# Optimization experiments

Measured on AMD Instinct MI355X. Metric: run time of the kernel, lower is better.

Reference implementation:

```python
import jax, jax.numpy as jnp
import numpy as np

B = 512          # batch
IN_UNITS = 8     # primary capsule dim
IN_CH = 1152     # number of primary capsules
NUM_UNITS = 10   # output capsules (classes)
UNIT_SIZE = 16   # output capsule dim
BETA = 1.45      # squash beta: 1.45 - 0.22*(ep_iter/total) with ep_iter = n_iter = 0
NUM_ROUTING = 3


def setup_inputs() -> dict:
    key = jax.random.key(0)
    k1, k2 = jax.random.split(key)
    x = jax.random.normal(k1, (B, IN_UNITS, IN_CH), dtype=jnp.float32)
    # W parameter: torch shape (1, in_channels, num_units, unit_size, in_units); drop leading 1
    W = jax.random.normal(k2, (IN_CH, NUM_UNITS, UNIT_SIZE, IN_UNITS), dtype=jnp.float32)
    return {"x": x, "W": W}


def _squash(s):
    # s: (B, num_units, unit_size). Torch squash sums dim=2 of (B,1,nu,us,1),
    # which is the num_units axis (axis=1 here). Faithful to source.
    mag_sq = jnp.sum(s * s, axis=1, keepdims=True)          # (B,1,us)
    mag = jnp.sqrt(mag_sq)
    return mag_sq / (BETA + mag_sq) * (s / mag)


def reference(x, W):
    # u_hat[b,i,j,u] = sum_k W[i,j,u,k] * x[b,k,i]
    u_hat = jnp.einsum('ijuk,bki->biju', W, x)               # (B, IN_CH, NUM_UNITS, UNIT_SIZE)
    b_ij = jnp.zeros((IN_CH, NUM_UNITS), dtype=x.dtype)
    v = None
    for _ in range(NUM_ROUTING):
        c = jax.nn.softmax(b_ij, axis=0)                     # softmax over in_channels (dim=1 in torch)
        s = jnp.einsum('ij,biju->bju', c, u_hat)             # (B, NUM_UNITS, UNIT_SIZE)
        v = _squash(s)
        # b update: agreement <u_hat, v>, averaged over batch
        b_ij = jnp.einsum('biju,bju->ij', u_hat, v) / u_hat.shape[0]
    # rearrange 'b c (g h) w -> b c g (h w)' with g=4, w=1 -> reshape (B, nu, 4, us//4)
    return v.reshape(v.shape[0], NUM_UNITS, 4, UNIT_SIZE // 4)
```

## Files before the change

### kernel.cpp

```cpp
#include <hip/hip_runtime.h>
#include <hip/hip_bf16.h>
#include <math.h>

#define B    512
#define INU  8
#define IC   1152
#define NU   10
#define US   16
#define JU   160
#define KI   9216
#define BETAC 1.45f
#define NSPLIT 32
#define KC 288

typedef __attribute__((ext_vector_type(8))) __bf16 bf16x8;
typedef __attribute__((ext_vector_type(4))) float floatx4;

static __device__ __forceinline__ unsigned short f2bf(float f) {
  unsigned u = __builtin_bit_cast(unsigned, f);
  u = (u + 0x7fffu + ((u >> 16) & 1u)) >> 16;
  return (unsigned short)u;
}
static __device__ __forceinline__ float bf2f(unsigned short h) {
  return __builtin_bit_cast(float, ((unsigned)h) << 16);
}
static __device__ __forceinline__ uint4 scale8(uint4 wv, float4 cA, float4 cB) {
  union { uint4 u; unsigned short s[8]; } in;
  in.u = wv;
  union { uint4 u; __hip_bfloat162 h[4]; } o;
  o.h[0] = __float22bfloat162_rn(make_float2(bf2f(in.s[0]) * cA.x, bf2f(in.s[1]) * cA.y));
  o.h[1] = __float22bfloat162_rn(make_float2(bf2f(in.s[2]) * cA.z, bf2f(in.s[3]) * cA.w));
  o.h[2] = __float22bfloat162_rn(make_float2(bf2f(in.s[4]) * cB.x, bf2f(in.s[5]) * cB.y));
  o.h[3] = __float22bfloat162_rn(make_float2(bf2f(in.s[6]) * cB.z, bf2f(in.s[7]) * cB.w));
  return o.u;
}

__global__ __launch_bounds__(256) void prep_kernel(
    const float* __restrict__ x, const float* __restrict__ W,
    unsigned short* __restrict__ xb, unsigned short* __restrict__ xT,
    unsigned short* __restrict__ Wt, unsigned short* __restrict__ Wc,
    float* __restrict__ Wr) {
  __shared__ float ts[32 * 322];
  int id = blockIdx.x;
  int t = threadIdx.x;
  if (id < 1152) {
    int k0 = (id % 144) * 64;
    int b0 = (id / 144) * 64;
#pragma unroll
    for (int r = 0; r < 16; ++r) {
      int idx = t + 256 * r;
      int br = idx >> 6, kc = idx & 63;
      float v = x[(size_t)(b0 + br) * KI + k0 + kc];
      ts[br * 65 + kc] = v;
      xb[(size_t)(b0 + br) * KI + k0 + kc] = f2bf(v);
    }
    __syncthreads();
#pragma unroll
    for (int r = 0; r < 8; ++r) {
      int idx = t + 256 * r;
      int kr = idx >> 5, bc = (idx & 31) * 2;
      unsigned lo = f2bf(ts[bc * 65 + kr]);
      unsigned hi = f2bf(ts[(bc + 1) * 65 + kr]);
      *(unsigned*)&xT[(size_t)(k0 + kr) * B + b0 + bc] = lo | (hi << 16);
    }
  } else {
    int wid = id - 1152;
    int i0 = (wid >> 2) * 32;
    int c0 = (wid & 3) * 320;
#pragma unroll
    for (int r = 0; r < 20; ++r) {
      int q = t + 256 * r;
      int il = q / 160, c = (q - il * 160) * 2;
      *(float2*)&ts[il * 322 + c] =
          *(const float2*)&W[(size_t)(i0 + il) * 1280 + c0 + c];
    }
    __syncthreads();
    {
      const float cinv = 1.0f / (float)IC;
      int il2 = (t & 15) * 2;
      for (int p = (t >> 4); p < 320; p += 16) {
        int c = c0 + p;
        int ju = c >> 3, k = c & 7;
        unsigned lo = f2bf(ts[il2 * 322 + p]);
        unsigned hi = f2bf(ts[(il2 + 1) * 322 + p]);
        *(unsigned*)&Wt[(size_t)ju * KI + k * IC + i0 + il2] = lo | (hi << 16);
        unsigned lo2 = f2bf(bf2f((unsigned short)lo) * cinv);
        unsigned hi2 = f2bf(bf2f((unsigned short)hi) * cinv);
        *(unsigned*)&Wc[(size_t)ju * KI + k * IC + i0 + il2] = lo2 | (hi2 << 16);
      }
    }
    int ju0 = c0 >> 3;
    for (int q = t; q < 8 * 32 * 40; q += 256) {
      int k = q / 1280;
      int il = (q / 40) & 31;
      int jl = q - (q / 40) * 40;
      Wr[((size_t)k * IC + i0 + il) * JU + ju0 + jl] = ts[il * 322 + jl * 8 + k];
    }
  }
}

__global__ __launch_bounds__(256) void s_gemm_mfma(
    const unsigned short* __restrict__ xb, const unsigned short* __restrict__ Wc,
    float* __restrict__ sp) {
  int b0 = blockIdx.x * 64;
  int kbase = blockIdx.y * KC;
  int j0 = blockIdx.z * 80;
  int t = threadIdx.x;
  int w = t >> 6, lane = t & 63, col = lane & 15, quad = lane >> 4;
  __shared__ unsigned short xs[2][64 * 40];
  __shared__ unsigned short ms[2][80 * 40];

  int xrow = t >> 2, xc = (t & 3) * 8;
  int mrow0 = t >> 2, mrow1 = 64 + (t >> 2);
  int mc = (t & 3) * 8;

  uint4 xv, m0, m1;
  auto prefetch = [&](int k0) {
    xv = *(const uint4*)&xb[(size_t)(b0 + xrow) * KI + k0 + xc];
    m0 = *(const uint4*)&Wc[(size_t)(j0 + mrow0) * KI + k0 + mc];
    if (t < 64) m1 = *(const uint4*)&Wc[(size_t)(j0 + mrow1) * KI + k0 + mc];
  };
  auto commit = [&](int pb) {
    *(uint4*)&xs[pb][xrow * 40 + xc] = xv;
    *(uint4*)&ms[pb][mrow0 * 40 + mc] = m0;
    if (t < 64) *(uint4*)&ms[pb][mrow1 * 40 + mc] = m1;
  };
  floatx4 acc[5];
#pragma unroll
  for (int jt = 0; jt < 5; ++jt) acc[jt] = (floatx4){0.f, 0.f, 0.f, 0.f};
  const int nsteps = KC >> 5;
  prefetch(kbase);
  commit(0);
  prefetch(kbase + 32);
  for (int s = 0; s < nsteps; ++s) {
    __syncthreads();
    if (s + 1 < nsteps) commit((s + 1) & 1);
    if (s + 2 < nsteps) prefetch(kbase + (s + 2) * 32);
    bf16x8 a = *(bf16x8*)&xs[s & 1][(w * 16 + col) * 40 + quad * 8];
#pragma unroll
    for (int jt = 0; jt < 5; ++jt) {
      bf16x8 bb = *(bf16x8*)&ms[s & 1][(jt * 16 + col) * 40 + quad * 8];
      acc[jt] = __builtin_amdgcn_mfma_f32_16x16x32_bf16(a, bb, acc[jt], 0, 0, 0);
    }
  }
#pragma unroll
  for (int jt = 0; jt < 5; ++jt)
#pragma unroll
    for (int r = 0; r < 4; ++r) {
      int b = b0 + w * 16 + quad * 4 + r;
      sp[((size_t)b * NSPLIT + blockIdx.y) * JU + j0 + jt * 16 + col] = acc[jt][r];
    }
}

__global__ __launch_bounds__(192) void squash_kernel(
    const float* __restrict__ sp, unsigned short* __restrict__ vT,
    float* __restrict__ out) {
  int b = blockIdx.x;
  int t = threadIdx.x;
  __shared__ float sv[JU];
  __shared__ float fac[US];
  float s = 0.0f;
  if (t < JU) {
#pragma unroll
    for (int k = 0; k < NSPLIT; ++k) s += sp[((size_t)b * NSPLIT + k) * JU + t];
    sv[t] = s;
  }
  __syncthreads();
  if (t < US) {
    float m = 0.0f;
#pragma unroll
    for (int j = 0; j < NU; ++j) {
      float q = sv[j * US + t];
      m += q * q;
    }
    fac[t] = sqrtf(m) / (BETAC + m);
  }
  __syncthreads();
  if (t < JU) {
    float val = s * fac[t & 15];
    vT[(size_t)t * B + b] = f2bf(val);
    if (out) out[(size_t)b * JU + t] = val;
  }
}

__global__ __launch_bounds__(256) void b_update_mfma(
    const unsigned short* __restrict__ xT, const unsigned short* __restrict__ vT,
    const float* __restrict__ Wr, float* __restrict__ bp) {
  int k = blockIdx.x / 18;
  int i0 = (blockIdx.x - k * 18) * 64;
  int bs = blockIdx.y;
  int j0 = blockIdx.z * 80;
  size_t ki0 = (size_t)k * IC + i0;
  int t = threadIdx.x;
  int w = t >> 6, lane = t & 63, col = lane & 15, quad = lane >> 4;
  __shared__ unsigned short xs[2][64 * 40];
  __shared__ unsigned short vs[2][80 * 40];
  int xrow = t >> 2, xc = (t & 3) * 8;
  int mrow0 = t >> 2, mrow1 = 64 + (t >> 2);
  int mc = (t & 3) * 8;
  uint4 xv, m0, m1;
  auto prefetch = [&](int c0) {
    xv = *(const uint4*)&xT[(ki0 + xrow) * B + c0 + xc];
    m0 = *(const uint4*)&vT[(size_t)(j0 + mrow0) * B + c0 + mc];
    if (t < 64) m1 = *(const uint4*)&vT[(size_t)(j0 + mrow1) * B + c0 + mc];
  };
  auto commit = [&](int pb) {
    *(uint4*)&xs[pb][xrow * 40 + xc] = xv;
    *(uint4*)&vs[pb][mrow0 * 40 + mc] = m0;
    if (t < 64) *(uint4*)&vs[pb][mrow1 * 40 + mc] = m1;
  };
  floatx4 acc[5];
#pragma unroll
  for (int jt = 0; jt < 5; ++jt) acc[jt] = (floatx4){0.f, 0.f, 0.f, 0.f};
  prefetch(bs * 256);
  commit(0);
  prefetch(bs * 256 + 32);
  for (int s = 0; s < 8; ++s) {
    __syncthreads();
    if (s + 1 < 8) commit((s + 1) & 1);
    if (s + 2 < 8) prefetch(bs * 256 + (s + 2) * 32);
    bf16x8 a = *(bf16x8*)&xs[s & 1][(w * 16 + col) * 40 + quad * 8];
#pragma unroll
    for (int jt = 0; jt < 5; ++jt) {
      bf16x8 bb = *(bf16x8*)&vs[s & 1][(jt * 16 + col) * 40 + quad * 8];
      acc[jt] = __builtin_amdgcn_mfma_f32_16x16x32_bf16(a, bb, acc[jt], 0, 0, 0);
    }
  }
  int p = k * 2 + bs;
  int jb = blockIdx.z * 5;
#pragma unroll
  for (int jt = 0; jt < 5; ++jt) {
#pragma unroll
    for (int r = 0; r < 4; ++r) {
      int i = i0 + w * 16 + quad * 4 + r;
      float wv = Wr[((size_t)k * IC + i) * JU + j0 + jt * 16 + col];
      float pr = wv * acc[jt][r];
      pr += __shfl_xor(pr, 1);
      pr += __shfl_xor(pr, 2);
      pr += __shfl_xor(pr, 4);
      pr += __shfl_xor(pr, 8);
      if (col == 0)
        bp[(size_t)p * (IC * NU) + (jb + jt) * IC + i] = pr * (1.0f / (float)B);
    }
  }
}

__global__ __launch_bounds__(256) void softmax_scale_kernel(
    const float* __restrict__ bp, const unsigned short* __restrict__ Wt,
    unsigned short* __restrict__ Wc) {
  int ju = blockIdx.x;
  int j = ju >> 4;
  int t = threadIdx.x;
  __shared__ float c[IC];
  __shared__ float red[256];
  for (int i = t; i < IC; i += 256) {
    float s = 0.0f;
#pragma unroll
    for (int p = 0; p < 16; ++p) s += bp[(size_t)p * (IC * NU) + j * IC + i];
    c[i] = s;
  }
  __syncthreads();
  float m = -1e30f;
  for (int i = t; i < IC; i += 256) m = fmaxf(m, c[i]);
  red[t] = m;
  __syncthreads();
  for (int o = 128; o > 0; o >>= 1) {
    if (t < o) red[t] = fmaxf(red[t], red[t + o]);
    __syncthreads();
  }
  float mx = red[0];
  __syncthreads();
  float sm = 0.0f;
  for (int i = t; i < IC; i += 256) {
    float e = __expf(c[i] - mx);
    c[i] = e;
    sm += e;
  }
  red[t] = sm;
  __syncthreads();
  for (int o = 128; o > 0; o >>= 1) {
    if (t < o) red[t] += red[t + o];
    __syncthreads();
  }
  float inv = 1.0f / red[0];
  for (int q = t; q < KI / 8; q += 256) {
    int ki = q * 8;
    int i = ki % IC;
    uint4 wv = *(const uint4*)&Wt[(size_t)ju * KI + ki];
    float4 cA = make_float4(c[i] * inv, c[i + 1] * inv, c[i + 2] * inv, c[i + 3] * inv);
    float4 cB = make_float4(c[i + 4] * inv, c[i + 5] * inv, c[i + 6] * inv, c[i + 7] * inv);
    *(uint4*)&Wc[(size_t)ju * KI + ki] = scale8(wv, cA, cB);
  }
}

extern "C" void kernel_launch(void* const* d_in, const int* in_sizes, int n_in,
                              void* d_out, int out_size, void* d_ws,
                              size_t ws_size, hipStream_t stream) {
  const float* x = (const float*)d_in[0];
  const float* W = (const float*)d_in[1];
  float* out = (float*)d_out;

  char* pws = (char*)d_ws;
  float* bp = (float*)pws;                     pws += (size_t)16 * IC * NU * 4;
  float* sp = (float*)pws;                     pws += (size_t)NSPLIT * B * JU * 4;
  float* Wr = (float*)pws;                     pws += (size_t)KI * JU * 4;
  unsigned short* xb = (unsigned short*)pws;   pws += (size_t)B * KI * 2;
  unsigned short* xT = (unsigned short*)pws;   pws += (size_t)KI * B * 2;
  unsigned short* Wt = (unsigned short*)pws;   pws += (size_t)JU * KI * 2;
  unsigned short* Wc = (unsigned short*)pws;   pws += (size_t)JU * KI * 2;
  unsigned short* vT = (unsigned short*)pws;

  prep_kernel<<<1152 + 144, 256, 0, stream>>>(x, W, xb, xT, Wt, Wc, Wr);

  for (int it = 0; it < 3; ++it) {
    s_gemm_mfma<<<dim3(8, NSPLIT, 2), 256, 0, stream>>>(xb, Wc, sp);
    squash_kernel<<<B, 192, 0, stream>>>(sp, vT, (it == 2) ? out : nullptr);
    if (it < 2) {
      b_update_mfma<<<dim3(144, 2, 2), 256, 0, stream>>>(xT, vT, Wr, bp);
      softmax_scale_kernel<<<160, 256, 0, stream>>>(bp, Wt, Wc);
    }
  }
}
```

Baseline: 158.9 us.

## Drop LDS staging in MFMA GEMMs, load fragments directly from global with register double-buffering

Both the s-GEMM and the b-update GEMM now have each wave load its MFMA operand fragments straight from global memory into registers, ping-ponging two register sets. This replaces the shared-memory double buffer and removes the __syncthreads barriers. The s-GEMM K split is also raised from 32 to 48 chunks to launch more blocks. The trade-off is that the W/v fragments are fetched redundantly by all four waves instead of once into LDS, and the squash stage must reduce more partial sums.

```diff
diff --git a/kernel.cpp b/kernel.cpp
--- a/kernel.cpp
+++ b/kernel.cpp
@@ -10,8 +10,8 @@
 #define JU   160
 #define KI   9216
 #define BETAC 1.45f
-#define NSPLIT 32
-#define KC 288
+#define NSPLIT 48
+#define KC 192
 
 typedef __attribute__((ext_vector_type(8))) __bf16 bf16x8;
 typedef __attribute__((ext_vector_type(4))) float floatx4;
@@ -102,52 +102,54 @@
 __global__ __launch_bounds__(256) void s_gemm_mfma(
     const unsigned short* __restrict__ xb, const unsigned short* __restrict__ Wc,
     float* __restrict__ sp) {
-  int b0 = blockIdx.x * 64;
-  int kbase = blockIdx.y * KC;
-  int j0 = blockIdx.z * 80;
-  int t = threadIdx.x;
-  int w = t >> 6, lane = t & 63, col = lane & 15, quad = lane >> 4;
-  __shared__ unsigned short xs[2][64 * 40];
-  __shared__ unsigned short ms[2][80 * 40];
-
-  int xrow = t >> 2, xc = (t & 3) * 8;
-  int mrow0 = t >> 2, mrow1 = 64 + (t >> 2);
-  int mc = (t & 3) * 8;
-
-  uint4 xv, m0, m1;
-  auto prefetch = [&](int k0) {
-    xv = *(const uint4*)&xb[(size_t)(b0 + xrow) * KI + k0 + xc];
-    m0 = *(const uint4*)&Wc[(size_t)(j0 + mrow0) * KI + k0 + mc];
-    if (t < 64) m1 = *(const uint4*)&Wc[(size_t)(j0 + mrow1) * KI + k0 + mc];
-  };
-  auto commit = [&](int pb) {
-    *(uint4*)&xs[pb][xrow * 40 + xc] = xv;
-    *(uint4*)&ms[pb][mrow0 * 40 + mc] = m0;
-    if (t < 64) *(uint4*)&ms[pb][mrow1 * 40 + mc] = m1;
-  };
+  const int t = threadIdx.x;
+  const int w = t >> 6, lane = t & 63, col = lane & 15, quad = lane >> 4;
+  const int b0 = blockIdx.x * 64 + w * 16;
+  const int k0 = blockIdx.y * KC;
+  const int j0 = blockIdx.z * 80;
+  const unsigned short* ax = xb + (size_t)(b0 + col) * KI + k0 + quad * 8;
+  const unsigned short* bw = Wc + (size_t)(j0 + col) * KI + k0 + quad * 8;
+
   floatx4 acc[5];
 #pragma unroll
   for (int jt = 0; jt < 5; ++jt) acc[jt] = (floatx4){0.f, 0.f, 0.f, 0.f};
-  const int nsteps = KC >> 5;
-  prefetch(kbase);
-  commit(0);
-  prefetch(kbase + 32);
-  for (int s = 0; s < nsteps; ++s) {
-    __syncthreads();
-    if (s + 1 < nsteps) commit((s + 1) & 1);
-    if (s + 2 < nsteps) prefetch(kbase + (s + 2) * 32);
-    bf16x8 a = *(bf16x8*)&xs[s & 1][(w * 16 + col) * 40 + quad * 8];
-#pragma unroll
-    for (int jt = 0; jt < 5; ++jt) {
-      bf16x8 bb = *(bf16x8*)&ms[s & 1][(jt * 16 + col) * 40 + quad * 8];
-      acc[jt] = __builtin_amdgcn_mfma_f32_16x16x32_bf16(a, bb, acc[jt], 0, 0, 0);
-    }
-  }
+
+  bf16x8 aA, aB, bA[5], bB[5];
+  aA = *(const bf16x8*)ax;
 #pragma unroll
   for (int jt = 0; jt < 5; ++jt)
+    bA[jt] = *(const bf16x8*)(bw + (size_t)jt * 16 * KI);
+
+  const int NSTEP = KC / 32;
+#pragma unroll
+  for (int s = 0; s < NSTEP; ++s) {
+    if ((s & 1) == 0) {
+      if (s + 1 < NSTEP) {
+        aB = *(const bf16x8*)(ax + (s + 1) * 32);
+#pragma unroll
+        for (int jt = 0; jt < 5; ++jt)
+          bB[jt] = *(const bf16x8*)(bw + (size_t)jt * 16 * KI + (s + 1) * 32);
+      }
+#pragma unroll
+      for (int jt = 0; jt < 5; ++jt)
+        acc[jt] = __builtin_amdgcn_mfma_f32_16x16x32_bf16(aA, bA[jt], acc[jt], 0, 0, 0);
+    } else {
+      if (s + 1 < NSTEP) {
+        aA = *(const bf16x8*)(ax + (s + 1) * 32);
+#pragma unroll
+        for (int jt = 0; jt < 5; ++jt)
+          bA[jt] = *(const bf16x8*)(bw + (size_t)jt * 16 * KI + (s + 1) * 32);
+      }
+#pragma unroll
+      for (int jt = 0; jt < 5; ++jt)
+        acc[jt] = __builtin_amdgcn_mfma_f32_16x16x32_bf16(aB, bB[jt], acc[jt], 0, 0, 0);
+    }
+  }
+#pragma unroll
+  for (int jt = 0; jt < 5; ++jt)
 #pragma unroll
     for (int r = 0; r < 4; ++r) {
-      int b = b0 + w * 16 + quad * 4 + r;
+      int b = b0 + quad * 4 + r;
       sp[((size_t)b * NSPLIT + blockIdx.y) * JU + j0 + jt * 16 + col] = acc[jt][r];
     }
 }
@@ -186,54 +188,59 @@
 __global__ __launch_bounds__(256) void b_update_mfma(
     const unsigned short* __restrict__ xT, const unsigned short* __restrict__ vT,
     const float* __restrict__ Wr, float* __restrict__ bp) {
-  int k = blockIdx.x / 18;
-  int i0 = (blockIdx.x - k * 18) * 64;
-  int bs = blockIdx.y;
-  int j0 = blockIdx.z * 80;
-  size_t ki0 = (size_t)k * IC + i0;
-  int t = threadIdx.x;
-  int w = t >> 6, lane = t & 63, col = lane & 15, quad = lane >> 4;
-  __shared__ unsigned short xs[2][64 * 40];
-  __shared__ unsigned short vs[2][80 * 40];
-  int xrow = t >> 2, xc = (t & 3) * 8;
-  int mrow0 = t >> 2, mrow1 = 64 + (t >> 2);
-  int mc = (t & 3) * 8;
-  uint4 xv, m0, m1;
-  auto prefetch = [&](int c0) {
-    xv = *(const uint4*)&xT[(ki0 + xrow) * B + c0 + xc];
-    m0 = *(const uint4*)&vT[(size_t)(j0 + mrow0) * B + c0 + mc];
-    if (t < 64) m1 = *(const uint4*)&vT[(size_t)(j0 + mrow1) * B + c0 + mc];
-  };
-  auto commit = [&](int pb) {
-    *(uint4*)&xs[pb][xrow * 40 + xc] = xv;
-    *(uint4*)&vs[pb][mrow0 * 40 + mc] = m0;
-    if (t < 64) *(uint4*)&vs[pb][mrow1 * 40 + mc] = m1;
-  };
+  const int t = threadIdx.x;
+  const int w = t >> 6, lane = t & 63, col = lane & 15, quad = lane >> 4;
+  const int kk = blockIdx.x / 18;
+  const int i0 = (blockIdx.x - kk * 18) * 64 + w * 16;
+  const int c0 = blockIdx.y * 256;
+  const int j0 = blockIdx.z * 80;
+  const unsigned short* ax = xT + ((size_t)kk * IC + i0 + col) * B + c0 + quad * 8;
+  const unsigned short* bv = vT + (size_t)(j0 + col) * B + c0 + quad * 8;
+
   floatx4 acc[5];
 #pragma unroll
   for (int jt = 0; jt < 5; ++jt) acc[jt] = (floatx4){0.f, 0.f, 0.f, 0.f};
-  prefetch(bs * 256);
-  commit(0);
-  prefetch(bs * 256 + 32);
-  for (int s = 0; s < 8; ++s) {
-    __syncthreads();
-    if (s + 1 < 8) commit((s + 1) & 1);
-    if (s + 2 < 8) prefetch(bs * 256 + (s + 2) * 32);
-    bf16x8 a = *(bf16x8*)&xs[s & 1][(w * 16 + col) * 40 + quad * 8];
-#pragma unroll
-    for (int jt = 0; jt < 5; ++jt) {
-      bf16x8 bb = *(bf16x8*)&vs[s & 1][(jt * 16 + col) * 40 + quad * 8];
-      acc[jt] = __builtin_amdgcn_mfma_f32_16x16x32_bf16(a, bb, acc[jt], 0, 0, 0);
-    }
-  }
-  int p = k * 2 + bs;
-  int jb = blockIdx.z * 5;
+
+  bf16x8 aA, aB, bA[5], bB[5];
+  aA = *(const bf16x8*)ax;
+#pragma unroll
+  for (int jt = 0; jt < 5; ++jt)
+    bA[jt] = *(const bf16x8*)(bv + (size_t)jt * 16 * B);
+
+  const int NSTEP = 8;
+#pragma unroll
+  for (int s = 0; s < NSTEP; ++s) {
+    if ((s & 1) == 0) {
+      if (s + 1 < NSTEP) {
+        aB = *(const bf16x8*)(ax + (s + 1) * 32);
+#pragma unroll
+        for (int jt = 0; jt < 5; ++jt)
+          bB[jt] = *(const bf16x8*)(bv + (size_t)jt * 16 * B + (s + 1) * 32);
+      }
+#pragma unroll
+      for (int jt = 0; jt < 5; ++jt)
+        acc[jt] = __builtin_amdgcn_mfma_f32_16x16x32_bf16(aA, bA[jt], acc[jt], 0, 0, 0);
+    } else {
+      if (s + 1 < NSTEP) {
+        aA = *(const bf16x8*)(ax + (s + 1) * 32);
+#pragma unroll
+        for (int jt = 0; jt < 5; ++jt)
+          bA[jt] = *(const bf16x8*)(bv + (size_t)jt * 16 * B + (s + 1) * 32);
+      }
+#pragma unroll
+      for (int jt = 0; jt < 5; ++jt)
+        acc[jt] = __builtin_amdgcn_mfma_f32_16x16x32_bf16(aB, bB[jt], acc[jt], 0, 0, 0);
+    }
+  }
+
+  const int p = kk * 2 + blockIdx.y;
+  const int jb = blockIdx.z * 5;
 #pragma unroll
   for (int jt = 0; jt < 5; ++jt) {
 #pragma unroll
     for (int r = 0; r < 4; ++r) {
-      int i = i0 + w * 16 + quad * 4 + r;
-      float wv = Wr[((size_t)k * IC + i) * JU + j0 + jt * 16 + col];
+      int i = i0 + quad * 4 + r;
+      float wv = Wr[((size_t)kk * IC + i) * JU + j0 + jt * 16 + col];
       float pr = wv * acc[jt][r];
       pr += __shfl_xor(pr, 1);
       pr += __shfl_xor(pr, 2);
```

Result: slower. 201.2 us (+26.6%).
